# Kernel optimization log

Hardware: AMD Instinct MI355X
Metric: run time of the kernel (lower is better)

Reference implementation:

```python
import jax, jax.numpy as jnp
import numpy as np

B, T, CIN, H, COUT, OUT_T = 512, 128, 64, 256, 64, 32


def setup_inputs() -> dict:
    key = jax.random.key(0)
    ks = jax.random.split(key, 12)
    s = lambda fan: 1.0 / np.sqrt(fan)
    return {
        "times": jnp.arange(T, dtype=jnp.float32),
        "coeffs": jax.random.normal(ks[0], (B, T, CIN), jnp.float32),
        "noise": jax.random.normal(ks[1], (T - 1, B, H), jnp.float32),
        # initial_network: Linear(input_channels, hidden_channels)
        "W_init": jax.random.normal(ks[2], (CIN, H), jnp.float32) * s(CIN),
        "b_init": jax.random.normal(ks[3], (H,), jnp.float32) * s(CIN),
        # SDE func drift / diffusion (diagonal noise)
        "Wf": jax.random.normal(ks[4], (H, H), jnp.float32) * s(H),
        "bf": jax.random.normal(ks[5], (H,), jnp.float32) * s(H),
        "Wg": jax.random.normal(ks[6], (H, H), jnp.float32) * s(H),
        "bg": jax.random.normal(ks[7], (H,), jnp.float32) * s(H),
        # head: Linear(H,H) -> ReLU -> Linear(H,COUT)
        "W1": jax.random.normal(ks[8], (H, H), jnp.float32) * s(H),
        "b1": jax.random.normal(ks[9], (H,), jnp.float32) * s(H),
        "W2": jax.random.normal(ks[10], (H, COUT), jnp.float32) * s(H),
        "b2": jax.random.normal(ks[11], (COUT,), jnp.float32) * s(H),
        "output_time": OUT_T,
    }


def reference(times, coeffs, noise, W_init, b_init, Wf, bf, Wg, bg, W1, b1, W2, b2, output_time):
    # dt = max(min(diff(times)), 0.001) as in the torch module
    dt = jnp.maximum(jnp.min(times[1:] - times[:-1]), 0.001)
    sqrt_dt = jnp.sqrt(dt)

    # z0 = initial_network(X.evaluate(times[0])) -> first control value
    x0 = coeffs[:, 0, :]                       # [B, CIN]
    z0 = x0 @ W_init + b_init                  # [B, H]

    def step(z, eps):
        f = jnp.tanh(z @ Wf + bf)              # drift
        g = jax.nn.sigmoid(z @ Wg + bg)        # diagonal diffusion
        z_next = z + f * dt + g * (sqrt_dt * eps)
        return z_next, z_next

    _, zs = jax.lax.scan(step, z0, noise)      # [T-1, B, H]
    z_t = jnp.concatenate([z0[None], zs], 0)   # [T, B, H]
    z_t = jnp.swapaxes(z_t, 0, 1)              # [B, T, H]  (transpose(0,1))

    h = z_t[:, z_t.shape[1] - output_time:, :] # [B, output_time, H]
    pred_y = jax.nn.relu(h @ W1 + b1) @ W2 + b2
    return pred_y
```

## Files before the change

kernel.cpp:

```cpp
#include <hip/hip_runtime.h>
#include <hip/hip_fp8.h>
#include <math.h>

#define B_      512
#define T_      128
#define CIN_    64
#define H_      256
#define COUT_   64
#define OUT_T_  32
#define NB_     16
#define NSTEP_  (T_ - 1)
#define HWIN_   (T_ - OUT_T_)
#define CUT_    63

#define INV16_  1.52587890625e-5f

typedef _Float16 half8  __attribute__((ext_vector_type(8)));
typedef float    floatx4 __attribute__((ext_vector_type(4)));
typedef long     longx2 __attribute__((ext_vector_type(2)));

#define LDS_TOTAL_ 152072

#define BARRIER_LGKM() asm volatile("s_waitcnt lgkmcnt(0)\n\ts_barrier" ::: "memory")

__device__ __forceinline__ float tanh_fast(float x){
  float e = __expf(2.0f * x);
  return 1.0f - 2.0f * __builtin_amdgcn_rcpf(e + 1.0f);
}
__device__ __forceinline__ float sigm_fast(float x){
  return __builtin_amdgcn_rcpf(1.0f + __expf(-x));
}
__device__ __forceinline__ int SWZ16(int r){ return ((r >> 2) & 3) << 4; }
__device__ __forceinline__ int SWZ8 (int r){ return ((r >> 2) & 3) << 5; }

__global__ void packFG_kernel(const float* __restrict__ W, _Float16* __restrict__ Ph,
                              unsigned char* __restrict__ P8){
  int i = blockIdx.x * blockDim.x + threadIdx.x;
  if (i >= H_ * H_) return;
  int k = i >> 8, n = i & 255;
  float w = W[i];
  _Float16 h = (_Float16)w;
  int off16 = (((n >> 5) * 16 + (k >> 5) * 2 + ((n >> 4) & 1)) << 10)
            + ((((k >> 3) & 3) * 16 + (n & 15)) << 4) + ((k & 7) << 1);
  *(_Float16*)((char*)Ph + off16) = h;
  int lanei = ((k >> 3) & 3) * 16 + (n & 15);
  int off8 = ((n >> 5) << 13) + ((k >> 5) << 10) + (lanei << 4)
           + (((n >> 4) & 1) << 3) + (k & 7);
  P8[off8] = __hip_cvt_float_to_fp8((w - (float)h) * 65536.0f,
                                    __HIP_SATFINITE, __HIP_E4M3);
}

__global__ void pack_kernel(const float* __restrict__ W, _Float16* __restrict__ Ph,
                            int K, int N){
  int i = blockIdx.x * blockDim.x + threadIdx.x;
  if (i >= K * N) return;
  int k = i / N, n = i - k * N;
  Ph[((k >> 5) * N + n) * 32 + (k & 31)] = (_Float16)W[i];
}

__global__ __launch_bounds__(512, 2) void scan_kernel(
    const float* __restrict__ times,
    const float* __restrict__ coeffs,
    const float* __restrict__ noise,
    const float* __restrict__ W_init,
    const float* __restrict__ b_init,
    const float* __restrict__ bf,
    const float* __restrict__ bg,
    const _Float16* __restrict__ WfPh,
    const _Float16* __restrict__ WgPh,
    const unsigned char* __restrict__ W8lF,
    const unsigned char* __restrict__ W8lG,
    _Float16* __restrict__ zhist)
{
  extern __shared__ __align__(16) char dynlds[];
  unsigned char* w8lds = (unsigned char*)dynlds;
  _Float16* zst   = (_Float16*)(dynlds + 131072);
  _Float16* zlt   = (_Float16*)(dynlds + 139264);
  unsigned char* z8t = (unsigned char*)(dynlds + 147456);
  float* diffs = (float*)(dynlds + 151552);
  float* dtsh  = (float*)(dynlds + 152064);
  float* x0_lds = (float*)(dynlds);
  float* z0f    = (float*)(dynlds + 4096);

  const int tid  = threadIdx.x;
  const int lane = tid & 63;
  const int wv   = tid >> 6;
  const int lo   = lane & 15;
  const int hi   = lane >> 4;
  const int b0   = blockIdx.x * NB_;

  if (tid < 127) diffs[tid] = times[tid + 1] - times[tid];
  if (tid == 127) diffs[127] = 3.4e38f;

  float bfv[2], bgv[2];
  #pragma unroll
  for (int t2 = 0; t2 < 2; ++t2){
    bfv[t2] = bf[32*wv + 16*t2 + lo];
    bgv[t2] = bg[32*wv + 16*t2 + lo];
  }

  for (int i = tid; i < NB_ * CIN_; i += 512)
    x0_lds[i] = coeffs[(size_t)(b0 + (i >> 6)) * (T_ * CIN_) + (i & 63)];
  __syncthreads();

  if (tid < 64){
    float m = fminf(diffs[tid], diffs[tid + 64]);
    #pragma unroll
    for (int o = 32; o; o >>= 1) m = fminf(m, __shfl_down(m, o, 64));
    if (tid == 0){
      float dt0 = fmaxf(m, 0.001f);
      dtsh[0] = dt0; dtsh[1] = sqrtf(dt0);
    }
  }

  {
    int r = tid & 15, c0 = (tid >> 4) * 8;
    float acc[8];
    #pragma unroll
    for (int j = 0; j < 8; ++j) acc[j] = b_init[c0 + j];
    for (int k = 0; k < CIN_; ++k){
      float x = x0_lds[r * CIN_ + k];
      const float* wrow = W_init + k * H_ + c0;
      #pragma unroll
      for (int j = 0; j < 8; ++j) acc[j] += x * wrow[j];
    }
    #pragma unroll
    for (int j = 0; j < 8; ++j) z0f[r * H_ + c0 + j] = acc[j];
  }
  __syncthreads();

  const float dt = dtsh[0], sqdt = dtsh[1];

  float zreg[2][4];
  #pragma unroll
  for (int t2 = 0; t2 < 2; ++t2){
    int col = 32*wv + 16*t2 + lo;
    #pragma unroll
    for (int rg = 0; rg < 4; ++rg)
      zreg[t2][rg] = z0f[(hi*4 + rg) * H_ + col];
  }
  for (int i = tid; i < NB_ * H_; i += 512){
    int rr = i >> 8;
    float zv = z0f[i];
    _Float16 zh = (_Float16)zv;
    int idx = i ^ SWZ16(rr);
    zst[idx] = zh;
    zlt[idx] = (_Float16)(zv - (float)zh);
    z8t[i ^ SWZ8(rr)] = __hip_cvt_float_to_fp8(zv, __HIP_SATFINITE, __HIP_E4M3);
  }
  __syncthreads();

  for (int i = tid * 16; i < 65536; i += 512 * 16){
    *(int4*)(w8lds + i)         = *(const int4*)(W8lF + i);
    *(int4*)(w8lds + 65536 + i) = *(const int4*)(W8lG + i);
  }
  __syncthreads();

  const int eb0 = (b0 + hi*4) * H_ + 32*wv + lo;
  const size_t zh0 = (size_t)(b0 + hi*4) * (OUT_T_ * H_) + 32*wv + lo;

  const int wb16 = (wv << 14) + (((hi << 4) + lo) << 4);
  const char* pfB = (const char*)WfPh + wb16;
  const char* pgB = (const char*)WgPh + wb16;
  const int w8b = (wv << 13) + (lane << 4);

  int aoff[8], a8off[8];
  #pragma unroll
  for (int kt = 0; kt < 8; ++kt){
    aoff[kt]  = (lo*H_ + kt*32 + hi*8) ^ SWZ16(lo);
    a8off[kt] = (lo*H_ + kt*32 + hi*8) ^ SWZ8(lo);
  }
  int woff[2][4], w8off_[2][4];
  #pragma unroll
  for (int t2 = 0; t2 < 2; ++t2)
    #pragma unroll
    for (int rg = 0; rg < 4; ++rg){
      int row = hi*4 + rg, col = 32*wv + 16*t2 + lo;
      woff[t2][rg]   = (row * H_ + col) ^ SWZ16(row);
      w8off_[t2][rg] = (row * H_ + col) ^ SWZ8(row);
    }

  floatx4 uF[2], uG[2], u8F[2], u8G[2];
  uF[0] = (floatx4){0.f,0.f,0.f,0.f}; uF[1] = uF[0];
  uG[0] = uF[0]; uG[1] = uF[0];
  u8F[0] = uF[0]; u8F[1] = uF[0]; u8G[0] = uF[0]; u8G[1] = uF[0];
  #pragma unroll
  for (int kt = 0; kt < 8; ++kt){
    half8 ah = *(const half8*)&zst[aoff[kt]];
    half8 al = *(const half8*)&zlt[aoff[kt]];
    long  a8 = *(const long*)&z8t[a8off[kt]];
    longx2 wf8 = *(const longx2*)(w8lds + w8b + (kt << 10));
    longx2 wg8 = *(const longx2*)(w8lds + 65536 + w8b + (kt << 10));
    #pragma unroll
    for (int t2 = 0; t2 < 2; ++t2){
      half8 whf = *(const half8*)(pfB + (kt*2 + t2)*1024);
      half8 whg = *(const half8*)(pgB + (kt*2 + t2)*1024);
      uF[t2]  = __builtin_amdgcn_mfma_f32_16x16x32_f16(ah, whf, uF[t2], 0,0,0);
      uF[t2]  = __builtin_amdgcn_mfma_f32_16x16x32_f16(al, whf, uF[t2], 0,0,0);
      uG[t2]  = __builtin_amdgcn_mfma_f32_16x16x32_f16(ah, whg, uG[t2], 0,0,0);
      uG[t2]  = __builtin_amdgcn_mfma_f32_16x16x32_f16(al, whg, uG[t2], 0,0,0);
      u8F[t2] = __builtin_amdgcn_mfma_f32_16x16x32_fp8_fp8(a8, wf8[t2], u8F[t2], 0,0,0);
      u8G[t2] = __builtin_amdgcn_mfma_f32_16x16x32_fp8_fp8(a8, wg8[t2], u8G[t2], 0,0,0);
    }
  }
  #pragma unroll
  for (int t2 = 0; t2 < 2; ++t2)
    #pragma unroll
    for (int rg = 0; rg < 4; ++rg){
      uF[t2][rg] += bfv[t2];
      uG[t2][rg] += bgv[t2];
    }

  const char* epp = (const char*)(noise + eb0);
  float eps[2][4];
  #pragma unroll
  for (int t2 = 0; t2 < 2; ++t2)
    #pragma unroll
    for (int rg = 0; rg < 4; ++rg)
      eps[t2][rg] = *(const float*)(epp + (rg*H_ + t2*16)*4);

  __syncthreads();

  unsigned int wlo = 0;

  for (int s = 0; s < NSTEP_; ++s){
    const bool full = (s < CUT_);
    const char* pf = pfB + wlo;
    const char* pg = pgB + wlo;

    #pragma unroll
    for (int t2 = 0; t2 < 2; ++t2){
      float dzv[4];
      #pragma unroll
      for (int rg = 0; rg < 4; ++rg){
        float uf = fmaf(INV16_, u8F[t2][rg], uF[t2][rg]);
        float ug = fmaf(INV16_, u8G[t2][rg], uG[t2][rg]);
        float f = tanh_fast(uf);
        float g = sigm_fast(ug);
        float dz = fmaf(g, sqdt * eps[t2][rg], f * dt);
        dzv[rg] = dz;
        zreg[t2][rg] += dz;
        _Float16 dh = (_Float16)dz;
        zst[woff[t2][rg]] = dh;
        if (full)
          zlt[woff[t2][rg]] = (_Float16)(dz - (float)dh);
      }
      if (full){
        int p01 = __builtin_amdgcn_cvt_pk_fp8_f32(dzv[0], dzv[1], 0, false);
        int p23 = __builtin_amdgcn_cvt_pk_fp8_f32(dzv[2], dzv[3], 0, false);
        z8t[w8off_[t2][0]] = (unsigned char)(p01);
        z8t[w8off_[t2][1]] = (unsigned char)(p01 >> 8);
        z8t[w8off_[t2][2]] = (unsigned char)(p23);
        z8t[w8off_[t2][3]] = (unsigned char)(p23 >> 8);
      }
    }

    if (s >= HWIN_ - 1){
      int sl = s - (HWIN_ - 1);
      #pragma unroll
      for (int t2 = 0; t2 < 2; ++t2)
        #pragma unroll
        for (int rg = 0; rg < 4; ++rg)
          zhist[zh0 + (size_t)rg*(OUT_T_*H_) + sl*H_ + t2*16] = (_Float16)zreg[t2][rg];
    }
    half8 whf[2][2], whg[2][2];
    if (s + 1 < NSTEP_){
      epp += (size_t)B_ * H_ * 4;
      #pragma unroll
      for (int t2 = 0; t2 < 2; ++t2)
        #pragma unroll
        for (int rg = 0; rg < 4; ++rg)
          eps[t2][rg] = *(const float*)(epp + (rg*H_ + t2*16)*4);
      #pragma unroll
      for (int kt = 0; kt < 2; ++kt)
        #pragma unroll
        for (int t2 = 0; t2 < 2; ++t2){
          whf[kt][t2] = *(const half8*)(pf + (kt*2 + t2)*1024);
          whg[kt][t2] = *(const half8*)(pg + (kt*2 + t2)*1024);
        }
    }

    BARRIER_LGKM();

    if (s + 1 < NSTEP_){
      if (full){
        #pragma unroll
        for (int kt = 0; kt < 8; ++kt){
          half8 ah = *(const half8*)&zst[aoff[kt]];
          half8 al = *(const half8*)&zlt[aoff[kt]];
          long  a8 = *(const long*)&z8t[a8off[kt]];
          longx2 wf8 = *(const longx2*)(w8lds + w8b + (kt << 10));
          longx2 wg8 = *(const longx2*)(w8lds + 65536 + w8b + (kt << 10));
          half8 f0 = whf[kt & 1][0], f1 = whf[kt & 1][1];
          half8 g0 = whg[kt & 1][0], g1 = whg[kt & 1][1];
          if (kt + 2 < 8){
            #pragma unroll
            for (int t2 = 0; t2 < 2; ++t2){
              whf[kt & 1][t2] = *(const half8*)(pf + ((kt+2)*2 + t2)*1024);
              whg[kt & 1][t2] = *(const half8*)(pg + ((kt+2)*2 + t2)*1024);
            }
          }
          uF[0]  = __builtin_amdgcn_mfma_f32_16x16x32_f16(ah, f0, uF[0], 0,0,0);
          uF[1]  = __builtin_amdgcn_mfma_f32_16x16x32_f16(ah, f1, uF[1], 0,0,0);
          uG[0]  = __builtin_amdgcn_mfma_f32_16x16x32_f16(ah, g0, uG[0], 0,0,0);
          uG[1]  = __builtin_amdgcn_mfma_f32_16x16x32_f16(ah, g1, uG[1], 0,0,0);
          uF[0]  = __builtin_amdgcn_mfma_f32_16x16x32_f16(al, f0, uF[0], 0,0,0);
          uF[1]  = __builtin_amdgcn_mfma_f32_16x16x32_f16(al, f1, uF[1], 0,0,0);
          uG[0]  = __builtin_amdgcn_mfma_f32_16x16x32_f16(al, g0, uG[0], 0,0,0);
          uG[1]  = __builtin_amdgcn_mfma_f32_16x16x32_f16(al, g1, uG[1], 0,0,0);
          u8F[0] = __builtin_amdgcn_mfma_f32_16x16x32_fp8_fp8(a8, wf8[0], u8F[0], 0,0,0);
          u8F[1] = __builtin_amdgcn_mfma_f32_16x16x32_fp8_fp8(a8, wf8[1], u8F[1], 0,0,0);
          u8G[0] = __builtin_amdgcn_mfma_f32_16x16x32_fp8_fp8(a8, wg8[0], u8G[0], 0,0,0);
          u8G[1] = __builtin_amdgcn_mfma_f32_16x16x32_fp8_fp8(a8, wg8[1], u8G[1], 0,0,0);
        }
      } else {
        #pragma unroll
        for (int kt = 0; kt < 8; ++kt){
          half8 ah = *(const half8*)&zst[aoff[kt]];
          half8 f0 = whf[kt & 1][0], f1 = whf[kt & 1][1];
          half8 g0 = whg[kt & 1][0], g1 = whg[kt & 1][1];
          if (kt + 2 < 8){
            #pragma unroll
            for (int t2 = 0; t2 < 2; ++t2){
              whf[kt & 1][t2] = *(const half8*)(pf + ((kt+2)*2 + t2)*1024);
              whg[kt & 1][t2] = *(const half8*)(pg + ((kt+2)*2 + t2)*1024);
            }
          }
          uF[0] = __builtin_amdgcn_mfma_f32_16x16x32_f16(ah, f0, uF[0], 0,0,0);
          uF[1] = __builtin_amdgcn_mfma_f32_16x16x32_f16(ah, f1, uF[1], 0,0,0);
          uG[0] = __builtin_amdgcn_mfma_f32_16x16x32_f16(ah, g0, uG[0], 0,0,0);
          uG[1] = __builtin_amdgcn_mfma_f32_16x16x32_f16(ah, g1, uG[1], 0,0,0);
        }
      }
    }

    BARRIER_LGKM();
    asm volatile("" : "+v"(wlo));
  }
}

__global__ __launch_bounds__(256) void head_kernel(
    const _Float16* __restrict__ zhist,
    const _Float16* __restrict__ W1P,
    const _Float16* __restrict__ W2P,
    const float* __restrict__ b1,
    const float* __restrict__ b2,
    float* __restrict__ out)
{
  __shared__ __align__(16) _Float16 hbuf[64 * H_];
  __shared__ __align__(16) _Float16 ubuf[64 * H_];

  const int tid  = threadIdx.x;
  const int lane = tid & 63;
  const int wv   = tid >> 6;
  const int lo   = lane & 15;
  const int hi   = lane >> 4;
  const int m0   = blockIdx.x * 64;

  for (int c = tid; c < 64 * 32; c += 256){
    int rr = c >> 5, c8 = (c & 31) * 8;
    *(half8*)&hbuf[(rr * H_ + c8) ^ ((rr & 7) << 3)] =
        *(const half8*)&zhist[(size_t)(m0 + rr) * H_ + c8];
  }

  half8 w1f[4][8];
  #pragma unroll
  for (int nt = 0; nt < 4; ++nt){
    int n0 = 64*wv + 16*nt + lo;
    #pragma unroll
    for (int kt = 0; kt < 8; ++kt)
      w1f[nt][kt] = *(const half8*)(W1P + (kt*H_ + n0)*32 + 8*hi);
  }
  half8 w2f[8];
  #pragma unroll
  for (int kt = 0; kt < 8; ++kt)
    w2f[kt] = *(const half8*)(W2P + (kt*COUT_ + 16*wv + lo)*32 + 8*hi);

  float b1v[4];
  #pragma unroll
  for (int nt = 0; nt < 4; ++nt) b1v[nt] = b1[64*wv + 16*nt + lo];
  float b2v = b2[16*wv + lo];

  __syncthreads();

  for (int mt = 0; mt < 4; ++mt){
    half8 a[8];
    #pragma unroll
    for (int kt = 0; kt < 8; ++kt)
      a[kt] = *(const half8*)&hbuf[((mt*16 + lo) * H_ + kt*32 + hi*8) ^ ((lo & 7) << 3)];
    #pragma unroll
    for (int nt = 0; nt < 4; ++nt){
      floatx4 acc = {0.f,0.f,0.f,0.f};
      #pragma unroll
      for (int kt = 0; kt < 8; ++kt)
        acc = __builtin_amdgcn_mfma_f32_16x16x32_f16(a[kt], w1f[nt][kt], acc, 0,0,0);
      #pragma unroll
      for (int rg = 0; rg < 4; ++rg){
        float u = fmaxf(acc[rg] + b1v[nt], 0.0f);
        int rr = mt*16 + hi*4 + rg;
        int cc = 64*wv + 16*nt + lo;
        ubuf[(rr * H_ + cc) ^ ((rr & 7) << 3)] = (_Float16)u;
      }
    }
  }
  __syncthreads();

  for (int mt = 0; mt < 4; ++mt){
    half8 a[8];
    #pragma unroll
    for (int kt = 0; kt < 8; ++kt)
      a[kt] = *(const half8*)&ubuf[((mt*16 + lo) * H_ + kt*32 + hi*8) ^ ((lo & 7) << 3)];
    floatx4 acc = {0.f,0.f,0.f,0.f};
    #pragma unroll
    for (int kt = 0; kt < 8; ++kt)
      acc = __builtin_amdgcn_mfma_f32_16x16x32_f16(a[kt], w2f[kt], acc, 0,0,0);
    #pragma unroll
    for (int rg = 0; rg < 4; ++rg)
      out[(size_t)(m0 + mt*16 + hi*4 + rg) * COUT_ + 16*wv + lo] = acc[rg] + b2v;
  }
}

extern "C" void kernel_launch(void* const* d_in, const int* in_sizes, int n_in,
                              void* d_out, int out_size, void* d_ws, size_t ws_size,
                              hipStream_t stream) {
  const float* times  = (const float*)d_in[0];
  const float* coeffs = (const float*)d_in[1];
  const float* noise  = (const float*)d_in[2];
  const float* W_init = (const float*)d_in[3];
  const float* b_init = (const float*)d_in[4];
  const float* Wf     = (const float*)d_in[5];
  const float* bf     = (const float*)d_in[6];
  const float* Wg     = (const float*)d_in[7];
  const float* bg     = (const float*)d_in[8];
  const float* W1     = (const float*)d_in[9];
  const float* b1     = (const float*)d_in[10];
  const float* W2     = (const float*)d_in[11];
  const float* b2     = (const float*)d_in[12];

  char* ws = (char*)d_ws;
  _Float16*      zhist = (_Float16*)(ws);
  _Float16*      WfPh  = (_Float16*)(ws + 8388608);
  _Float16*      WgPh  = (_Float16*)(ws + 8519680);
  unsigned char* W8lF  = (unsigned char*)(ws + 8650752);
  unsigned char* W8lG  = (unsigned char*)(ws + 8716288);
  _Float16*      W1Ph  = (_Float16*)(ws + 8781824);
  _Float16*      W2Ph  = (_Float16*)(ws + 8978432);

  packFG_kernel<<<(H_*H_ + 255)/256, 256, 0, stream>>>(Wf, WfPh, W8lF);
  packFG_kernel<<<(H_*H_ + 255)/256, 256, 0, stream>>>(Wg, WgPh, W8lG);
  pack_kernel<<<(H_*H_ + 255)/256, 256, 0, stream>>>(W1, W1Ph, H_, H_);
  pack_kernel<<<(H_*COUT_ + 255)/256, 256, 0, stream>>>(W2, W2Ph, H_, COUT_);

  hipFuncSetAttribute((const void*)scan_kernel,
                      hipFuncAttributeMaxDynamicSharedMemorySize, LDS_TOTAL_);
  scan_kernel<<<B_ / NB_, 512, LDS_TOTAL_, stream>>>(
      times, coeffs, noise, W_init, b_init, bf, bg,
      WfPh, WgPh, W8lF, W8lG, zhist);

  head_kernel<<<(B_ * OUT_T_) / 64, 256, 0, stream>>>(zhist, W1Ph, W2Ph, b1, b2,
                                                      (float*)d_out);
}
```

Baseline: 449.7 us.

## Peel SDE step loop and double-buffer reduced-precision phase to drop a barrier

Splits the time-step loop into a full-precision phase (f16 hi/lo plus fp8 correction) and a reduced phase, removing the per-step `full` branching. In the reduced phase the z tile alternates between the zst and zlt LDS buffers, so the trailing barrier can go and only one barrier per step remains. The weight-fragment prefetch depth also grows from 2 to 4 k-tiles. The cost is more live VGPRs for prefetched weights, which could reduce occupancy or cause spills, and correctness relies on the double-buffer ordering across steps.

```diff
diff --git a/kernel.cpp b/kernel.cpp
--- a/kernel.cpp
+++ b/kernel.cpp
@@ -223,8 +223,7 @@
 
   unsigned int wlo = 0;
 
-  for (int s = 0; s < NSTEP_; ++s){
-    const bool full = (s < CUT_);
+  for (int s = 0; s < CUT_; ++s){
     const char* pf = pfB + wlo;
     const char* pg = pgB + wlo;
 
@@ -242,18 +241,84 @@
         zreg[t2][rg] += dz;
         _Float16 dh = (_Float16)dz;
         zst[woff[t2][rg]] = dh;
-        if (full)
-          zlt[woff[t2][rg]] = (_Float16)(dz - (float)dh);
-      }
-      if (full){
-        int p01 = __builtin_amdgcn_cvt_pk_fp8_f32(dzv[0], dzv[1], 0, false);
-        int p23 = __builtin_amdgcn_cvt_pk_fp8_f32(dzv[2], dzv[3], 0, false);
-        z8t[w8off_[t2][0]] = (unsigned char)(p01);
-        z8t[w8off_[t2][1]] = (unsigned char)(p01 >> 8);
-        z8t[w8off_[t2][2]] = (unsigned char)(p23);
-        z8t[w8off_[t2][3]] = (unsigned char)(p23 >> 8);
-      }
-    }
+        zlt[woff[t2][rg]] = (_Float16)(dz - (float)dh);
+      }
+      int p01 = __builtin_amdgcn_cvt_pk_fp8_f32(dzv[0], dzv[1], 0, false);
+      int p23 = __builtin_amdgcn_cvt_pk_fp8_f32(dzv[2], dzv[3], 0, false);
+      z8t[w8off_[t2][0]] = (unsigned char)(p01);
+      z8t[w8off_[t2][1]] = (unsigned char)(p01 >> 8);
+      z8t[w8off_[t2][2]] = (unsigned char)(p23);
+      z8t[w8off_[t2][3]] = (unsigned char)(p23 >> 8);
+    }
+
+    epp += (size_t)B_ * H_ * 4;
+    #pragma unroll
+    for (int t2 = 0; t2 < 2; ++t2)
+      #pragma unroll
+      for (int rg = 0; rg < 4; ++rg)
+        eps[t2][rg] = *(const float*)(epp + (rg*H_ + t2*16)*4);
+    half8 whf[2][2], whg[2][2];
+    #pragma unroll
+    for (int kt = 0; kt < 2; ++kt)
+      #pragma unroll
+      for (int t2 = 0; t2 < 2; ++t2){
+        whf[kt][t2] = *(const half8*)(pf + (kt*2 + t2)*1024);
+        whg[kt][t2] = *(const half8*)(pg + (kt*2 + t2)*1024);
+      }
+
+    BARRIER_LGKM();
+
+    #pragma unroll
+    for (int kt = 0; kt < 8; ++kt){
+      half8 ah = *(const half8*)&zst[aoff[kt]];
+      half8 al = *(const half8*)&zlt[aoff[kt]];
+      long  a8 = *(const long*)&z8t[a8off[kt]];
+      longx2 wf8 = *(const longx2*)(w8lds + w8b + (kt << 10));
+      longx2 wg8 = *(const longx2*)(w8lds + 65536 + w8b + (kt << 10));
+      half8 f0 = whf[kt & 1][0], f1 = whf[kt & 1][1];
+      half8 g0 = whg[kt & 1][0], g1 = whg[kt & 1][1];
+      if (kt + 2 < 8){
+        #pragma unroll
+        for (int t2 = 0; t2 < 2; ++t2){
+          whf[kt & 1][t2] = *(const half8*)(pf + ((kt+2)*2 + t2)*1024);
+          whg[kt & 1][t2] = *(const half8*)(pg + ((kt+2)*2 + t2)*1024);
+        }
+      }
+      uF[0]  = __builtin_amdgcn_mfma_f32_16x16x32_f16(ah, f0, uF[0], 0,0,0);
+      uF[1]  = __builtin_amdgcn_mfma_f32_16x16x32_f16(ah, f1, uF[1], 0,0,0);
+      uG[0]  = __builtin_amdgcn_mfma_f32_16x16x32_f16(ah, g0, uG[0], 0,0,0);
+      uG[1]  = __builtin_amdgcn_mfma_f32_16x16x32_f16(ah, g1, uG[1], 0,0,0);
+      uF[0]  = __builtin_amdgcn_mfma_f32_16x16x32_f16(al, f0, uF[0], 0,0,0);
+      uF[1]  = __builtin_amdgcn_mfma_f32_16x16x32_f16(al, f1, uF[1], 0,0,0);
+      uG[0]  = __builtin_amdgcn_mfma_f32_16x16x32_f16(al, g0, uG[0], 0,0,0);
+      uG[1]  = __builtin_amdgcn_mfma_f32_16x16x32_f16(al, g1, uG[1], 0,0,0);
+      u8F[0] = __builtin_amdgcn_mfma_f32_16x16x32_fp8_fp8(a8, wf8[0], u8F[0], 0,0,0);
+      u8F[1] = __builtin_amdgcn_mfma_f32_16x16x32_fp8_fp8(a8, wf8[1], u8F[1], 0,0,0);
+      u8G[0] = __builtin_amdgcn_mfma_f32_16x16x32_fp8_fp8(a8, wg8[0], u8G[0], 0,0,0);
+      u8G[1] = __builtin_amdgcn_mfma_f32_16x16x32_fp8_fp8(a8, wg8[1], u8G[1], 0,0,0);
+    }
+
+    BARRIER_LGKM();
+    asm volatile("" : "+v"(wlo));
+  }
+
+  for (int s = CUT_; s < NSTEP_; ++s){
+    _Float16* zw = (s & 1) ? zlt : zst;
+    const char* pf = pfB + wlo;
+    const char* pg = pgB + wlo;
+
+    #pragma unroll
+    for (int t2 = 0; t2 < 2; ++t2)
+      #pragma unroll
+      for (int rg = 0; rg < 4; ++rg){
+        float uf = fmaf(INV16_, u8F[t2][rg], uF[t2][rg]);
+        float ug = fmaf(INV16_, u8G[t2][rg], uG[t2][rg]);
+        float f = tanh_fast(uf);
+        float g = sigm_fast(ug);
+        float dz = fmaf(g, sqdt * eps[t2][rg], f * dt);
+        zreg[t2][rg] += dz;
+        zw[woff[t2][rg]] = (_Float16)dz;
+      }
 
     if (s >= HWIN_ - 1){
       int sl = s - (HWIN_ - 1);
@@ -263,7 +328,8 @@
         for (int rg = 0; rg < 4; ++rg)
           zhist[zh0 + (size_t)rg*(OUT_T_*H_) + sl*H_ + t2*16] = (_Float16)zreg[t2][rg];
     }
-    half8 whf[2][2], whg[2][2];
+
+    half8 whf[4][2], whg[4][2];
     if (s + 1 < NSTEP_){
       epp += (size_t)B_ * H_ * 4;
       #pragma unroll
@@ -272,7 +338,7 @@
         for (int rg = 0; rg < 4; ++rg)
           eps[t2][rg] = *(const float*)(epp + (rg*H_ + t2*16)*4);
       #pragma unroll
-      for (int kt = 0; kt < 2; ++kt)
+      for (int kt = 0; kt < 4; ++kt)
         #pragma unroll
         for (int t2 = 0; t2 < 2; ++t2){
           whf[kt][t2] = *(const half8*)(pf + (kt*2 + t2)*1024);
@@ -283,58 +349,24 @@
     BARRIER_LGKM();
 
     if (s + 1 < NSTEP_){
-      if (full){
-        #pragma unroll
-        for (int kt = 0; kt < 8; ++kt){
-          half8 ah = *(const half8*)&zst[aoff[kt]];
-          half8 al = *(const half8*)&zlt[aoff[kt]];
-          long  a8 = *(const long*)&z8t[a8off[kt]];
-          longx2 wf8 = *(const longx2*)(w8lds + w8b + (kt << 10));
-          longx2 wg8 = *(const longx2*)(w8lds + 65536 + w8b + (kt << 10));
-          half8 f0 = whf[kt & 1][0], f1 = whf[kt & 1][1];
-          half8 g0 = whg[kt & 1][0], g1 = whg[kt & 1][1];
-          if (kt + 2 < 8){
-            #pragma unroll
-            for (int t2 = 0; t2 < 2; ++t2){
-              whf[kt & 1][t2] = *(const half8*)(pf + ((kt+2)*2 + t2)*1024);
-              whg[kt & 1][t2] = *(const half8*)(pg + ((kt+2)*2 + t2)*1024);
-            }
+      #pragma unroll
+      for (int kt = 0; kt < 8; ++kt){
+        half8 ah = *(const half8*)&zw[aoff[kt]];
+        half8 f0 = whf[kt & 3][0], f1 = whf[kt & 3][1];
+        half8 g0 = whg[kt & 3][0], g1 = whg[kt & 3][1];
+        if (kt + 4 < 8){
+          #pragma unroll
+          for (int t2 = 0; t2 < 2; ++t2){
+            whf[kt & 3][t2] = *(const half8*)(pf + ((kt+4)*2 + t2)*1024);
+            whg[kt & 3][t2] = *(const half8*)(pg + ((kt+4)*2 + t2)*1024);
           }
-          uF[0]  = __builtin_amdgcn_mfma_f32_16x16x32_f16(ah, f0, uF[0], 0,0,0);
-          uF[1]  = __builtin_amdgcn_mfma_f32_16x16x32_f16(ah, f1, uF[1], 0,0,0);
-          uG[0]  = __builtin_amdgcn_mfma_f32_16x16x32_f16(ah, g0, uG[0], 0,0,0);
-          uG[1]  = __builtin_amdgcn_mfma_f32_16x16x32_f16(ah, g1, uG[1], 0,0,0);
-          uF[0]  = __builtin_amdgcn_mfma_f32_16x16x32_f16(al, f0, uF[0], 0,0,0);
-          uF[1]  = __builtin_amdgcn_mfma_f32_16x16x32_f16(al, f1, uF[1], 0,0,0);
-          uG[0]  = __builtin_amdgcn_mfma_f32_16x16x32_f16(al, g0, uG[0], 0,0,0);
-          uG[1]  = __builtin_amdgcn_mfma_f32_16x16x32_f16(al, g1, uG[1], 0,0,0);
-          u8F[0] = __builtin_amdgcn_mfma_f32_16x16x32_fp8_fp8(a8, wf8[0], u8F[0], 0,0,0);
-          u8F[1] = __builtin_amdgcn_mfma_f32_16x16x32_fp8_fp8(a8, wf8[1], u8F[1], 0,0,0);
-          u8G[0] = __builtin_amdgcn_mfma_f32_16x16x32_fp8_fp8(a8, wg8[0], u8G[0], 0,0,0);
-          u8G[1] = __builtin_amdgcn_mfma_f32_16x16x32_fp8_fp8(a8, wg8[1], u8G[1], 0,0,0);
         }
-      } else {
-        #pragma unroll
-        for (int kt = 0; kt < 8; ++kt){
-          half8 ah = *(const half8*)&zst[aoff[kt]];
-          half8 f0 = whf[kt & 1][0], f1 = whf[kt & 1][1];
-          half8 g0 = whg[kt & 1][0], g1 = whg[kt & 1][1];
-          if (kt + 2 < 8){
-            #pragma unroll
-            for (int t2 = 0; t2 < 2; ++t2){
-              whf[kt & 1][t2] = *(const half8*)(pf + ((kt+2)*2 + t2)*1024);
-              whg[kt & 1][t2] = *(const half8*)(pg + ((kt+2)*2 + t2)*1024);
-            }
-          }
-          uF[0] = __builtin_amdgcn_mfma_f32_16x16x32_f16(ah, f0, uF[0], 0,0,0);
-          uF[1] = __builtin_amdgcn_mfma_f32_16x16x32_f16(ah, f1, uF[1], 0,0,0);
-          uG[0] = __builtin_amdgcn_mfma_f32_16x16x32_f16(ah, g0, uG[0], 0,0,0);
-          uG[1] = __builtin_amdgcn_mfma_f32_16x16x32_f16(ah, g1, uG[1], 0,0,0);
-        }
-      }
-    }
-
-    BARRIER_LGKM();
+        uF[0] = __builtin_amdgcn_mfma_f32_16x16x32_f16(ah, f0, uF[0], 0,0,0);
+        uF[1] = __builtin_amdgcn_mfma_f32_16x16x32_f16(ah, f1, uF[1], 0,0,0);
+        uG[0] = __builtin_amdgcn_mfma_f32_16x16x32_f16(ah, g0, uG[0], 0,0,0);
+        uG[1] = __builtin_amdgcn_mfma_f32_16x16x32_f16(ah, g1, uG[1], 0,0,0);
+      }
+    }
     asm volatile("" : "+v"(wlo));
   }
 }
```

New measurement: 402.1 us. 1.12x faster.
